# Optimization experiments

Hardware: AMD Instinct MI355X
Metric: run time of the kernel (lower is better)

## Reference

```python
import jax, jax.numpy as jnp
import numpy as np

K, NC, NA = 9, 13, 5
NB, NH, NW = 128, 26, 26
NT, L = 50, 2 * K + 3
NOOBJ, OBJ, SIL = 1.0, 5.0, 0.6
COORD_S, CLASS_S = 1.0, 1.0
PRETRAIN_EPOCHS = 15
TH, SHARP = 80.0, 2.0                      # corner-conf distance threshold (px), sharpness
SCALE = np.array([640.0, 480.0], np.float32)  # im_width, im_height used by corner_confidences
CONF0 = float(np.exp(SHARP) - 1.0)
ANCHORS = np.array([1.482, 2.2412, 2.0501, 3.1265, 2.3946, 4.6891,
                    3.1018, 3.991, 3.4879, 5.8851], np.float32).reshape(NA, 2)


def setup_inputs():
    k1, k2 = jax.random.split(jax.random.key(0))
    output = jax.random.normal(k1, (NB, NA * (2 * K + 1 + NC), NH, NW), dtype=jnp.float32)
    target = jax.random.uniform(k2, (NB, NT * L), dtype=jnp.float32)
    return {"output": output, "target": target, "epoch": 20}


def _corner_conf(pred, gt):
    # pred, gt: [..., K, 2] normalized corners -> mean per-corner confidence [...]
    d = jnp.sqrt((((pred - gt) * jnp.asarray(SCALE)) ** 2).sum(-1))  # pixel distance [..., K]
    c = (jnp.exp(SHARP * (1.0 - d / TH)) - 1.0) / CONF0
    return jnp.where(d < TH, c, 0.0).mean(-1)


def _region_loss(output, target, epoch):
    nAnch, nPix = NA * NH * NW, NH * NW
    tgt = jax.lax.stop_gradient(target).reshape(NB, NT, L)
    out = output.reshape(NB, NA, 2 * K + 1 + NC, NH, NW)
    # keypoint 0 gets sigmoid, the rest are raw offsets
    xs = jnp.concatenate([jax.nn.sigmoid(out[:, :, 0:1]), out[:, :, 2:2 * K:2]], axis=2)  # [B,A,K,H,W]
    ys = jnp.concatenate([jax.nn.sigmoid(out[:, :, 1:2]), out[:, :, 3:2 * K:2]], axis=2)
    conf = jax.nn.sigmoid(out[:, :, 2 * K])                             # [B,A,H,W]
    cls_logits = jnp.transpose(out[:, :, 2 * K + 1:], (0, 1, 3, 4, 2))  # [B,A,H,W,NC]

    gxg = jnp.arange(NW, dtype=jnp.float32)
    gyg = jnp.arange(NH, dtype=jnp.float32)
    px = (jax.lax.stop_gradient(xs) + gxg) / NW            # detached, as torch uses .data
    py = (jax.lax.stop_gradient(ys) + gyg[:, None]) / NH
    # pred corners per anchor cell, flat anchor index = a*H*W + j*W + i -> [B, A*H*W, K, 2]
    pc = jnp.transpose(jnp.stack([px, py], -1), (0, 1, 3, 4, 2, 5)).reshape(NB, nAnch, K, 2)

    gt_xy = tgt[:, :, 1:1 + 2 * K].reshape(NB, NT, K, 2)
    # torch loop breaks at first target with x1 == 0 -> cumulative validity
    valid = jnp.cumprod((tgt[:, :, 1] != 0).astype(jnp.int32), axis=1) > 0  # [B,T]

    # pass 1: max corner confidence over valid GT, per anchor cell
    def max_conf_step(cur, inp):
        gt_t, v_t = inp                                    # [B,K,2], [B]
        c = _corner_conf(pc, gt_t[:, None]).reshape(NB, NA, NH, NW)
        return jnp.where(v_t[:, None, None, None], jnp.maximum(cur, c), cur), None

    cur_confs, _ = jax.lax.scan(max_conf_step, jnp.zeros((NB, NA, NH, NW), jnp.float32),
                                (jnp.swapaxes(gt_xy, 0, 1), valid.T))
    conf_mask0 = jnp.where(cur_confs > SIL, 0.0, NOOBJ)

    # per-target quantities (vectorized over b,t)
    gx = gt_xy[..., 0] * NW                                # [B,T,K]
    gy = gt_xy[..., 1] * NH
    gi0 = jnp.clip(jnp.floor(gx[:, :, 0]).astype(jnp.int32), 0, NW - 1)  # [B,T]
    gj0 = jnp.clip(jnp.floor(gy[:, :, 0]).astype(jnp.int32), 0, NH - 1)
    # pred_box is fetched with best_n == -1 (as in the source); emulate torch negative flat index via mod
    flat_idx = jnp.mod(jnp.arange(NB)[:, None] * nAnch - nPix + gj0 * NW + gi0, NB * nAnch)
    pred_box = pc.reshape(NB * nAnch, K, 2)[flat_idx]      # [B,T,K,2]
    conf_t = _corner_conf(pred_box, gt_xy)                 # [B,T]
    gw = tgt[:, :, L - 2] * NW
    gh = tgt[:, :, L - 1] * NH
    aw, ah = ANCHORS[:, 0], ANCHORS[:, 1]
    mw = jnp.minimum(aw, gw[..., None])                    # centered-box IoU (bbox_iou, cxcywh)
    mh = jnp.minimum(ah, gh[..., None])
    inter = mw * mh
    iou = inter / (aw * ah + (gw * gh)[..., None] - inter)
    best_n = jnp.argmax(iou, axis=-1).astype(jnp.int32)    # [B,T] (first max, like strict '>')
    txv = gx - gi0[..., None].astype(jnp.float32)          # [B,T,K]
    tyv = gy - gj0[..., None].astype(jnp.float32)
    tclsv = tgt[:, :, 0]

    # pass 2: sequential scatter matching torch overwrite order over t
    barange = jnp.arange(NB)
    z = jnp.zeros((NB, NA, NH, NW), jnp.float32)
    zk = jnp.zeros((NB, NA, NH, NW, K), jnp.float32)

    def scatter_step(carry, inp):
        cm, clm, cfm, tx, ty, tcf, tcl = carry
        v, bn, gj, gi, cft, txt, tyt, tct = inp
        idx = (barange, bn, gj, gi)
        vk = v[:, None]
        cm = cm.at[idx].set(jnp.where(v, 1.0, cm[idx]))
        clm = clm.at[idx].set(jnp.where(v, 1.0, clm[idx]))
        cfm = cfm.at[idx].set(jnp.where(v, OBJ, cfm[idx]))
        tx = tx.at[idx].set(jnp.where(vk, txt, tx[idx]))
        ty = ty.at[idx].set(jnp.where(vk, tyt, ty[idx]))
        tcf = tcf.at[idx].set(jnp.where(v, cft, tcf[idx]))
        tcl = tcl.at[idx].set(jnp.where(v, tct, tcl[idx]))
        return (cm, clm, cfm, tx, ty, tcf, tcl), None

    inps = (valid.T, best_n.T, gj0.T, gi0.T, conf_t.T,
            jnp.swapaxes(txv, 0, 1), jnp.swapaxes(tyv, 0, 1), tclsv.T)
    (coord_mask, cls_mask, conf_mask, tx, ty, tconf, tcls), _ = jax.lax.scan(
        scatter_step, (z, z, conf_mask0, zk, zk, z, z), inps)

    # losses
    xsT = jnp.transpose(xs, (0, 1, 3, 4, 2))               # [B,A,H,W,K]
    ysT = jnp.transpose(ys, (0, 1, 3, 4, 2))
    cmk = coord_mask[..., None]
    loss_x = 0.5 * COORD_S * jnp.sum(((xsT - tx) * cmk) ** 2)
    loss_y = 0.5 * COORD_S * jnp.sum(((ysT - ty) * cmk) ** 2)
    sq = jnp.sqrt(conf_mask)
    loss_conf = 0.5 * jnp.sum(((conf - tconf) * sq) ** 2)
    labels = jnp.clip(tcls.astype(jnp.int32), 0, NC - 1)
    ce = -jnp.take_along_axis(jax.nn.log_softmax(cls_logits, axis=-1),
                              labels[..., None], axis=-1)[..., 0]
    loss_cls = CLASS_S * jnp.sum(ce * cls_mask)
    loss = loss_x + loss_y + loss_cls
    if epoch > PRETRAIN_EPOCHS:
        loss = loss + loss_conf
    return loss


def reference(output, target, epoch):
    return _region_loss(output, target, epoch)
```

## Files before the change

### kernel.cpp

```cpp
#include <hip/hip_runtime.h>
#include <math.h>

#define KK     9
#define NCLS   13
#define NANC   5
#define NBB    128
#define NHH    26
#define NWW    26
#define NTT    50
#define LL     21
#define CHC    32
#define NPIX   676
#define NANCHT 3380
#define NCELLT 432640
#define GTS    20
#define MWPB   106

#define LOG2E_F   1.4426950408889634f
#define K1C       2.8853900817779268f
#define K2C       0.036067376022224085f
#define SXW       24.615384615384617f
#define SYH       18.461538461538463f
#define THRESH_S  43.500902934225507f
#define CONF_T_SCALE 0.017390849194407297f
#define OBJ_W     5.0f
#define EPOCH_PRETRAIN 15
#define BIGV      6.0e18f

#define CULL_H2   0.36f
#define HSCALE    0.03125f

typedef __attribute__((ext_vector_type(2))) float f2;
typedef __attribute__((ext_vector_type(2))) _Float16 h2;
typedef __attribute__((ext_vector_type(4))) unsigned int u4;

static __device__ __forceinline__ float fast_exp2(float x){
  return __builtin_amdgcn_exp2f(x);
}
static __device__ __forceinline__ float fast_sqrt(float x){
  return __builtin_amdgcn_sqrtf(x);
}
static __device__ __forceinline__ float sigmoidf_(float x){
  return 1.0f/(1.0f + fast_exp2(-LOG2E_F*x));
}

__constant__ float c_anch[10] = {1.482f,2.2412f,2.0501f,3.1265f,2.3946f,4.6891f,
                                 3.1018f,3.991f,3.4879f,5.8851f};


__global__ __launch_bounds__(64) void prep_kernel(const float* __restrict__ tgt,
                                                  float* __restrict__ gts_neg,
                                                  int* __restrict__ nvalid){
  int b = blockIdx.x;
  int t = threadIdx.x;
  const float* trow = tgt + (size_t)b*NTT*LL;
  float v1 = (t < NTT) ? trow[t*LL + 1] : 0.0f;
  unsigned long long mk = __ballot(t < NTT && v1 != 0.0f);
  int firstInvalid = __ffsll(~mk) - 1;
  if (t == 0) nvalid[b] = firstInvalid;
  for (int idx = t; idx < NTT*GTS; idx += 64){
    int tt = idx / GTS;
    int c  = idx - tt*GTS;
    float v;
    if (c == 9 || c == 19)      v = BIGV;
    else if (c < 9)             v = -(trow[tt*LL + 1 + 2*c] * 640.0f);
    else                        v = -(trow[tt*LL + 2 + 2*(c-10)] * 480.0f);
    gts_neg[(size_t)b*NTT*GTS + idx] = v;
  }
}

__global__ __launch_bounds__(256) void region_confmask_kernel(
    const float* __restrict__ outp, const float* __restrict__ gts_neg,
    const int* __restrict__ nvalid, unsigned int* __restrict__ maskw,
    double* __restrict__ partials){
  int b = blockIdx.y;
  int cell = blockIdx.x * blockDim.x + threadIdx.x;

  __shared__ float sgt[NTT*GTS] __attribute__((aligned(16)));
  __shared__ h2   sgth[NTT*12] __attribute__((aligned(16)));
  const float* g32 = gts_neg + (size_t)b*NTT*GTS;
  for (int idx = threadIdx.x; idx < NTT*GTS; idx += 256)
    sgt[idx] = g32[idx];
  for (int widx = threadIdx.x; widx < NTT*12; widx += 256){
    int tt = widx / 12, w = widx - tt*12;
    float a0 = BIGV, a1 = BIGV;
    if (w < 10){ a0 = g32[tt*GTS + 2*w]; a1 = g32[tt*GTS + 2*w + 1]; }
    h2 hh;
    hh.x = (_Float16)(a0 * HSCALE);
    hh.y = (_Float16)(a1 * HSCALE);
    sgth[widx] = hh;
  }
  __syncthreads();

  int m0 = 1;
  float contrib = 0.0f;
  if (cell < NANCHT){
    int a   = cell / NPIX;
    int rem = cell - a*NPIX;
    int j   = rem / NWW;
    int i   = rem - j*NWW;
    const float* base = outp + (((size_t)b*NANC + a)*CHC)*NPIX + rem;

    f2 Pxp[5], Pyp[5];
#pragma unroll
    for (int k = 0; k < KK; ++k){
      float rx = base[(2*k)*NPIX];
      float ry = base[(2*k+1)*NPIX];
      if (k == 0){ rx = sigmoidf_(rx); ry = sigmoidf_(ry); }
      Pxp[k>>1][k&1] = (rx + (float)i) * SXW;
      Pyp[k>>1][k&1] = (ry + (float)j) * SYH;
    }
    Pxp[4][1] = 0.0f; Pyp[4][1] = 0.0f;

    h2 Pxh[5], Pyh[5];
#pragma unroll
    for (int p = 0; p < 5; ++p){
      Pxh[p].x = (_Float16)(Pxp[p].x * HSCALE);
      Pxh[p].y = (_Float16)(Pxp[p].y * HSCALE);
      Pyh[p].x = (_Float16)(Pyp[p].x * HSCALE);
      Pyh[p].y = (_Float16)(Pyp[p].y * HSCALE);
    }

    int nv = nvalid[b];
    const _Float16 thh = (_Float16)CULL_H2;
    unsigned long long qbits = 0ull;
#pragma unroll 2
    for (int t = 0; t < nv; ++t){
      const u4* gh = (const u4*)(sgth + t*12);
      u4 q0 = gh[0], q1 = gh[1], q2 = gh[2];
      h2 Xa[5] = { __builtin_bit_cast(h2, q0.x), __builtin_bit_cast(h2, q0.y),
                   __builtin_bit_cast(h2, q0.z), __builtin_bit_cast(h2, q0.w),
                   __builtin_bit_cast(h2, q1.x) };
      h2 Ya[5] = { __builtin_bit_cast(h2, q1.y), __builtin_bit_cast(h2, q1.z),
                   __builtin_bit_cast(h2, q1.w), __builtin_bit_cast(h2, q2.x),
                   __builtin_bit_cast(h2, q2.y) };
      h2 m2 = {(_Float16)60000.0f, (_Float16)60000.0f};
#pragma unroll
      for (int p = 0; p < 5; ++p){
        h2 dx = Pxh[p] + Xa[p];
        h2 dy = Pyh[p] + Ya[p];
        h2 r  = __builtin_elementwise_fma(dy, dy, dx*dx);
        m2 = __builtin_elementwise_min(m2, r);
      }
      if (m2.x < thh || m2.y < thh) qbits |= (1ull << t);
    }

    if (__any(qbits != 0ull)){
      bool exc = false;
      while (qbits){
        int t = __ffsll((long long)qbits) - 1;
        qbits &= qbits - 1;
        const float* gg = sgt + t*GTS;
        float s = 0.0f;
#pragma unroll
        for (int k = 0; k < KK; ++k){
          float dx = Pxp[k>>1][k&1] + gg[k];
          float dy = Pyp[k>>1][k&1] + gg[10+k];
          float d  = fast_sqrt(fmaf(dy, dy, dx*dx));
          float e  = fast_exp2(fmaf(d, -K2C, K1C));
          s += fmaxf(e, 1.0f);
        }
        exc |= (s > THRESH_S);
      }
      if (exc) m0 = 0;
    }
    float cf = sigmoidf_(base[(2*KK)*NPIX]);
    contrib = m0 ? 0.5f*cf*cf : 0.0f;
  }

  unsigned long long mb = __ballot(m0 != 0);
  int lane = threadIdx.x & 63;
  int wavebase = blockIdx.x * 256 + (threadIdx.x & ~63);
  if ((lane & 31) == 0 && wavebase < NANCHT){
    unsigned int w = (lane == 0) ? (unsigned int)mb : (unsigned int)(mb >> 32);
    maskw[(size_t)b*MWPB + (wavebase >> 5) + (lane >> 5)] = w;
  }

#pragma unroll
  for (int o = 32; o > 0; o >>= 1) contrib += __shfl_xor(contrib, o, 64);
  __shared__ float wsum[4];
  int wid = threadIdx.x >> 6;
  if (lane == 0) wsum[wid] = contrib;
  __syncthreads();
  if (threadIdx.x == 0){
    double tot = (double)wsum[0] + (double)wsum[1] + (double)wsum[2] + (double)wsum[3];
    partials[blockIdx.y * gridDim.x + blockIdx.x] = tot;
  }
}

__global__ __launch_bounds__(64) void scatter_loss_kernel(
    const float* __restrict__ outp, const float* __restrict__ tgt,
    const int* __restrict__ nvalid, const unsigned int* __restrict__ maskw,
    double* __restrict__ bc_part){
  int b = blockIdx.x;
  int t = threadIdx.x;
  __shared__ int keys[NTT];
  int nv = nvalid[b];
  bool valid = (t < nv);

  int key = -1, gi0 = 0, gj0 = 0, bn = 0;
  float txv[KK], tyv[KK];
  float conf_t = 0.0f, tcls = 0.0f;

  if (t < NTT){
    const float* trow = tgt + ((size_t)b*NTT + t)*LL;
    tcls = trow[0];
    float gx0 = trow[1]*(float)NWW;
    float gy0 = trow[2]*(float)NHH;
    gi0 = min(max((int)floorf(gx0), 0), NWW-1);
    gj0 = min(max((int)floorf(gy0), 0), NHH-1);
#pragma unroll
    for (int k = 0; k < KK; ++k){
      txv[k] = trow[1+2*k]*(float)NWW - (float)gi0;
      tyv[k] = trow[2+2*k]*(float)NHH - (float)gj0;
    }
    float gw = trow[LL-2]*(float)NWW, gh = trow[LL-1]*(float)NHH;
    float best = -1.0f;
    for (int a = 0; a < NANC; ++a){
      float aw = c_anch[2*a], ah = c_anch[2*a+1];
      float inter = fminf(aw, gw) * fminf(ah, gh);
      float iou = inter / (aw*ah + gw*gh - inter);
      if (iou > best){ best = iou; bn = a; }
    }
    key = bn*NPIX + gj0*NWW + gi0;
    keys[t] = key;

    long f = (long)b*NANCHT - NPIX + gj0*NWW + gi0;
    if (f < 0) f += NCELLT;
    int bb  = (int)(f / NANCHT);
    int rr  = (int)(f - (long)bb*NANCHT);
    int aa  = rr / NPIX;
    int rr2 = rr - aa*NPIX;
    int jj  = rr2 / NWW;
    int ii  = rr2 - jj*NWW;
    const float* pbase = outp + (((size_t)bb*NANC + aa)*CHC)*NPIX + rr2;
    float s = 0.0f;
#pragma unroll
    for (int k = 0; k < KK; ++k){
      float rx = pbase[(2*k)*NPIX], ry = pbase[(2*k+1)*NPIX];
      if (k == 0){ rx = sigmoidf_(rx); ry = sigmoidf_(ry); }
      float Pxx = (rx + (float)ii)*SXW, Pyy = (ry + (float)jj)*SYH;
      float dx = Pxx - trow[1+2*k]*640.0f;
      float dy = Pyy - trow[2+2*k]*480.0f;
      float d  = fast_sqrt(fmaf(dy, dy, dx*dx));
      float e  = fast_exp2(fmaf(d, -K2C, K1C));
      s += fmaxf(e, 1.0f);
    }
    conf_t = (s - 9.0f) * CONF_T_SCALE;
  }
  __syncthreads();

  bool winner = valid;
  if (valid){
    for (int u = t+1; u < nv; ++u) if (keys[u] == key){ winner = false; break; }
  }

  double lx = 0.0, ly = 0.0, lcls = 0.0, lcf = 0.0;
  if (winner){
    const float* cbase = outp + (((size_t)b*NANC + bn)*CHC)*NPIX + gj0*NWW + gi0;
    float sx = 0.0f, sy = 0.0f;
#pragma unroll
    for (int k = 0; k < KK; ++k){
      float rx = cbase[(2*k)*NPIX], ry = cbase[(2*k+1)*NPIX];
      if (k == 0){ rx = sigmoidf_(rx); ry = sigmoidf_(ry); }
      float dx = rx - txv[k], dy = ry - tyv[k];
      sx = fmaf(dx, dx, sx); sy = fmaf(dy, dy, sy);
    }
    lx = 0.5*(double)sx; ly = 0.5*(double)sy;

    float lg[NCLS], mx = -1e30f;
#pragma unroll
    for (int c = 0; c < NCLS; ++c){ lg[c] = cbase[(2*KK+1+c)*NPIX]; mx = fmaxf(mx, lg[c]); }
    float se = 0.0f;
#pragma unroll
    for (int c = 0; c < NCLS; ++c) se += fast_exp2((lg[c]-mx)*LOG2E_F);
    int label = min(max((int)tcls, 0), NCLS-1);
    lcls = (double)(mx + logf(se) - lg[label]);

    float cf = sigmoidf_(cbase[(2*KK)*NPIX]);
    int idx = bn*NPIX + gj0*NWW + gi0;
    int m0 = (maskw[(size_t)b*MWPB + (idx >> 5)] >> (idx & 31)) & 1;
    float dcf = cf - conf_t;
    lcf = 0.5*OBJ_W*(double)(dcf*dcf) - (m0 ? 0.5*(double)(cf*cf) : 0.0);
  }

#pragma unroll
  for (int o = 32; o > 0; o >>= 1){
    lx  += __shfl_xor(lx,  o, 64);
    ly  += __shfl_xor(ly,  o, 64);
    lcls+= __shfl_xor(lcls,o, 64);
    lcf += __shfl_xor(lcf, o, 64);
  }
  if (threadIdx.x == 0){
    double* bp = bc_part + (size_t)b*4;
    bp[0] = lx; bp[1] = ly; bp[2] = lcls; bp[3] = lcf;
  }
}

__global__ __launch_bounds__(256) void finalize_kernel(
    const double* __restrict__ bc_part, const double* __restrict__ partials,
    const int* __restrict__ epoch_p, float* __restrict__ outv){
  int tid = threadIdx.x;
  double vx=0, vy=0, vc=0, vf=0, vb=0;
  for (int i = tid; i < NBB; i += 256){
    vx += bc_part[4*i]; vy += bc_part[4*i+1];
    vc += bc_part[4*i+2]; vf += bc_part[4*i+3];
  }
  for (int i = tid; i < 14*NBB; i += 256) vb += partials[i];
#pragma unroll
  for (int o = 32; o > 0; o >>= 1){
    vx += __shfl_xor(vx, o, 64); vy += __shfl_xor(vy, o, 64);
    vc += __shfl_xor(vc, o, 64); vf += __shfl_xor(vf, o, 64);
    vb += __shfl_xor(vb, o, 64);
  }
  __shared__ double sm[5][4];
  int wid = tid >> 6, lane = tid & 63;
  if (lane == 0){ sm[0][wid]=vx; sm[1][wid]=vy; sm[2][wid]=vc; sm[3][wid]=vf; sm[4][wid]=vb; }
  __syncthreads();
  if (tid == 0){
    double fx=0, fy=0, fc=0, ff=0, fb=0;
    for (int w = 0; w < 4; ++w){ fx+=sm[0][w]; fy+=sm[1][w]; fc+=sm[2][w]; ff+=sm[3][w]; fb+=sm[4][w]; }
    double loss = fx + fy + fc;
    if (*epoch_p > EPOCH_PRETRAIN) loss += ff + fb;
    outv[0] = (float)loss;
  }
}

extern "C" void kernel_launch(void* const* d_in, const int* in_sizes, int n_in,
                              void* d_out, int out_size, void* d_ws, size_t ws_size,
                              hipStream_t stream){
  (void)in_sizes; (void)n_in; (void)out_size; (void)ws_size;
  const float* outp = (const float*)d_in[0];
  const float* tgt  = (const float*)d_in[1];
  const int*   ep   = (const int*)d_in[2];
  float* outv = (float*)d_out;
  char* ws = (char*)d_ws;

  double* bc_part  = (double*)(ws);
  double* partials = (double*)(ws + 4096);
  float*  gts_neg  = (float*) (ws + 18432);
  int*    nvalid   = (int*)   (ws + 530432);
  unsigned int* maskw = (unsigned int*)(ws + 530944);

  prep_kernel<<<dim3(NBB), dim3(64), 0, stream>>>(tgt, gts_neg, nvalid);
  region_confmask_kernel<<<dim3(14, NBB), dim3(256), 0, stream>>>(outp, gts_neg, nvalid, maskw, partials);
  scatter_loss_kernel<<<dim3(NBB), dim3(64), 0, stream>>>(outp, tgt, nvalid, maskw, bc_part);
  finalize_kernel<<<dim3(1), dim3(256), 0, stream>>>(bc_part, partials, ep, outv);
}
```

Measured before the change: 134.5 us.

## Precompute fp16 GT table in prep and read it via scalar constant loads

After: 139.5 us. 3.8% more time.

```diff
diff --git a/kernel.cpp b/kernel.cpp
--- a/kernel.cpp
+++ b/kernel.cpp
@@ -1,5 +1,6 @@
 #include <hip/hip_runtime.h>
 #include <math.h>
+#include <stdint.h>
 
 #define KK     9
 #define NCLS   13
@@ -15,6 +16,7 @@
 #define NCELLT 432640
 #define GTS    20
 #define MWPB   106
+#define GTH_W  12
 
 #define LOG2E_F   1.4426950408889634f
 #define K1C       2.8853900817779268f
@@ -33,6 +35,7 @@
 typedef __attribute__((ext_vector_type(2))) float f2;
 typedef __attribute__((ext_vector_type(2))) _Float16 h2;
 typedef __attribute__((ext_vector_type(4))) unsigned int u4;
+typedef __attribute__((ext_vector_type(2))) unsigned int u2;
 
 static __device__ __forceinline__ float fast_exp2(float x){
   return __builtin_amdgcn_exp2f(x);
@@ -44,12 +47,20 @@
   return 1.0f/(1.0f + fast_exp2(-LOG2E_F*x));
 }
 
+static __device__ __forceinline__ u4 sload_u4(const unsigned int* p){
+  return *(const __attribute__((address_space(4))) u4*)(uintptr_t)p;
+}
+static __device__ __forceinline__ u2 sload_u2(const unsigned int* p){
+  return *(const __attribute__((address_space(4))) u2*)(uintptr_t)p;
+}
+
 __constant__ float c_anch[10] = {1.482f,2.2412f,2.0501f,3.1265f,2.3946f,4.6891f,
                                  3.1018f,3.991f,3.4879f,5.8851f};
 
 
 __global__ __launch_bounds__(64) void prep_kernel(const float* __restrict__ tgt,
                                                   float* __restrict__ gts_neg,
+                                                  unsigned int* __restrict__ gth,
                                                   int* __restrict__ nvalid){
   int b = blockIdx.x;
   int t = threadIdx.x;
@@ -67,106 +78,116 @@
     else                        v = -(trow[tt*LL + 2 + 2*(c-10)] * 480.0f);
     gts_neg[(size_t)b*NTT*GTS + idx] = v;
   }
+  for (int idx = t; idx < NTT*GTH_W; idx += 64){
+    int tt = idx / GTH_W;
+    int w  = idx - tt*GTH_W;
+    const float* tr2 = trow + tt*LL;
+    float a0 = BIGV, a1 = BIGV;
+    if (w < 5){
+      int k0 = 2*w;
+      a0 = -(tr2[1 + 2*k0] * 20.0f);
+      if (k0 + 1 < KK) a1 = -(tr2[1 + 2*(k0+1)] * 20.0f);
+    } else if (w < 10){
+      int k0 = 2*(w-5);
+      a0 = -(tr2[2 + 2*k0] * 15.0f);
+      if (k0 + 1 < KK) a1 = -(tr2[2 + 2*(k0+1)] * 15.0f);
+    }
+    h2 hh; hh.x = (_Float16)a0; hh.y = (_Float16)a1;
+    gth[(size_t)b*NTT*GTH_W + idx] = __builtin_bit_cast(unsigned int, hh);
+  }
 }
 
 __global__ __launch_bounds__(256) void region_confmask_kernel(
     const float* __restrict__ outp, const float* __restrict__ gts_neg,
+    const unsigned int* __restrict__ gth,
     const int* __restrict__ nvalid, unsigned int* __restrict__ maskw,
     double* __restrict__ partials){
   int b = blockIdx.y;
   int cell = blockIdx.x * blockDim.x + threadIdx.x;
+  bool live = (cell < NANCHT);
+  int cellc = live ? cell : (NANCHT-1);
 
   __shared__ float sgt[NTT*GTS] __attribute__((aligned(16)));
-  __shared__ h2   sgth[NTT*12] __attribute__((aligned(16)));
   const float* g32 = gts_neg + (size_t)b*NTT*GTS;
   for (int idx = threadIdx.x; idx < NTT*GTS; idx += 256)
     sgt[idx] = g32[idx];
-  for (int widx = threadIdx.x; widx < NTT*12; widx += 256){
-    int tt = widx / 12, w = widx - tt*12;
-    float a0 = BIGV, a1 = BIGV;
-    if (w < 10){ a0 = g32[tt*GTS + 2*w]; a1 = g32[tt*GTS + 2*w + 1]; }
-    h2 hh;
-    hh.x = (_Float16)(a0 * HSCALE);
-    hh.y = (_Float16)(a1 * HSCALE);
-    sgth[widx] = hh;
-  }
   __syncthreads();
 
+  int a   = cellc / NPIX;
+  int rem = cellc - a*NPIX;
+  int j   = rem / NWW;
+  int i   = rem - j*NWW;
+  const float* base = outp + (((size_t)b*NANC + a)*CHC)*NPIX + rem;
+
+  f2 Pxp[5], Pyp[5];
+#pragma unroll
+  for (int k = 0; k < KK; ++k){
+    float rx = base[(2*k)*NPIX];
+    float ry = base[(2*k+1)*NPIX];
+    if (k == 0){ rx = sigmoidf_(rx); ry = sigmoidf_(ry); }
+    Pxp[k>>1][k&1] = (rx + (float)i) * SXW;
+    Pyp[k>>1][k&1] = (ry + (float)j) * SYH;
+  }
+  Pxp[4][1] = 0.0f; Pyp[4][1] = 0.0f;
+
+  h2 Pxh[5], Pyh[5];
+#pragma unroll
+  for (int p = 0; p < 5; ++p){
+    Pxh[p].x = (_Float16)(Pxp[p].x * HSCALE);
+    Pxh[p].y = (_Float16)(Pxp[p].y * HSCALE);
+    Pyh[p].x = (_Float16)(Pyp[p].x * HSCALE);
+    Pyh[p].y = (_Float16)(Pyp[p].y * HSCALE);
+  }
+
+  int nv = nvalid[b];
+  const unsigned int* gthb = gth + (size_t)b*NTT*GTH_W;
+  const _Float16 thh = (_Float16)CULL_H2;
+  unsigned long long qbits = 0ull;
+#pragma unroll 2
+  for (int t = 0; t < nv; ++t){
+    u4 q0 = sload_u4(gthb + t*GTH_W);
+    u4 q1 = sload_u4(gthb + t*GTH_W + 4);
+    u2 q2 = sload_u2(gthb + t*GTH_W + 8);
+    h2 Xa[5] = { __builtin_bit_cast(h2, q0.x), __builtin_bit_cast(h2, q0.y),
+                 __builtin_bit_cast(h2, q0.z), __builtin_bit_cast(h2, q0.w),
+                 __builtin_bit_cast(h2, q1.x) };
+    h2 Ya[5] = { __builtin_bit_cast(h2, q1.y), __builtin_bit_cast(h2, q1.z),
+                 __builtin_bit_cast(h2, q1.w), __builtin_bit_cast(h2, q2.x),
+                 __builtin_bit_cast(h2, q2.y) };
+    h2 m2 = {(_Float16)60000.0f, (_Float16)60000.0f};
+#pragma unroll
+    for (int p = 0; p < 5; ++p){
+      h2 dx = Pxh[p] + Xa[p];
+      h2 dy = Pyh[p] + Ya[p];
+      h2 r  = __builtin_elementwise_fma(dy, dy, dx*dx);
+      m2 = __builtin_elementwise_min(m2, r);
+    }
+    _Float16 mm = (m2.x < m2.y) ? m2.x : m2.y;
+    if (mm < thh) qbits |= (1ull << t);
+  }
+
   int m0 = 1;
-  float contrib = 0.0f;
-  if (cell < NANCHT){
-    int a   = cell / NPIX;
-    int rem = cell - a*NPIX;
-    int j   = rem / NWW;
-    int i   = rem - j*NWW;
-    const float* base = outp + (((size_t)b*NANC + a)*CHC)*NPIX + rem;
-
-    f2 Pxp[5], Pyp[5];
-#pragma unroll
-    for (int k = 0; k < KK; ++k){
-      float rx = base[(2*k)*NPIX];
-      float ry = base[(2*k+1)*NPIX];
-      if (k == 0){ rx = sigmoidf_(rx); ry = sigmoidf_(ry); }
-      Pxp[k>>1][k&1] = (rx + (float)i) * SXW;
-      Pyp[k>>1][k&1] = (ry + (float)j) * SYH;
-    }
-    Pxp[4][1] = 0.0f; Pyp[4][1] = 0.0f;
-
-    h2 Pxh[5], Pyh[5];
-#pragma unroll
-    for (int p = 0; p < 5; ++p){
-      Pxh[p].x = (_Float16)(Pxp[p].x * HSCALE);
-      Pxh[p].y = (_Float16)(Pxp[p].y * HSCALE);
-      Pyh[p].x = (_Float16)(Pyp[p].x * HSCALE);
-      Pyh[p].y = (_Float16)(Pyp[p].y * HSCALE);
-    }
-
-    int nv = nvalid[b];
-    const _Float16 thh = (_Float16)CULL_H2;
-    unsigned long long qbits = 0ull;
-#pragma unroll 2
-    for (int t = 0; t < nv; ++t){
-      const u4* gh = (const u4*)(sgth + t*12);
-      u4 q0 = gh[0], q1 = gh[1], q2 = gh[2];
-      h2 Xa[5] = { __builtin_bit_cast(h2, q0.x), __builtin_bit_cast(h2, q0.y),
-                   __builtin_bit_cast(h2, q0.z), __builtin_bit_cast(h2, q0.w),
-                   __builtin_bit_cast(h2, q1.x) };
-      h2 Ya[5] = { __builtin_bit_cast(h2, q1.y), __builtin_bit_cast(h2, q1.z),
-                   __builtin_bit_cast(h2, q1.w), __builtin_bit_cast(h2, q2.x),
-                   __builtin_bit_cast(h2, q2.y) };
-      h2 m2 = {(_Float16)60000.0f, (_Float16)60000.0f};
-#pragma unroll
-      for (int p = 0; p < 5; ++p){
-        h2 dx = Pxh[p] + Xa[p];
-        h2 dy = Pyh[p] + Ya[p];
-        h2 r  = __builtin_elementwise_fma(dy, dy, dx*dx);
-        m2 = __builtin_elementwise_min(m2, r);
+  if (__any(qbits != 0ull)){
+    bool exc = false;
+    while (qbits){
+      int t = __ffsll((long long)qbits) - 1;
+      qbits &= qbits - 1;
+      const float* gg = sgt + t*GTS;
+      float s = 0.0f;
+#pragma unroll
+      for (int k = 0; k < KK; ++k){
+        float dx = Pxp[k>>1][k&1] + gg[k];
+        float dy = Pyp[k>>1][k&1] + gg[10+k];
+        float d  = fast_sqrt(fmaf(dy, dy, dx*dx));
+        float e  = fast_exp2(fmaf(d, -K2C, K1C));
+        s += fmaxf(e, 1.0f);
       }
-      if (m2.x < thh || m2.y < thh) qbits |= (1ull << t);
-    }
-
-    if (__any(qbits != 0ull)){
-      bool exc = false;
-      while (qbits){
-        int t = __ffsll((long long)qbits) - 1;
-        qbits &= qbits - 1;
-        const float* gg = sgt + t*GTS;
-        float s = 0.0f;
-#pragma unroll
-        for (int k = 0; k < KK; ++k){
-          float dx = Pxp[k>>1][k&1] + gg[k];
-          float dy = Pyp[k>>1][k&1] + gg[10+k];
-          float d  = fast_sqrt(fmaf(dy, dy, dx*dx));
-          float e  = fast_exp2(fmaf(d, -K2C, K1C));
-          s += fmaxf(e, 1.0f);
-        }
-        exc |= (s > THRESH_S);
-      }
-      if (exc) m0 = 0;
-    }
-    float cf = sigmoidf_(base[(2*KK)*NPIX]);
-    contrib = m0 ? 0.5f*cf*cf : 0.0f;
-  }
+      exc |= (s > THRESH_S);
+    }
+    if (exc) m0 = 0;
+  }
+  float cf = sigmoidf_(base[(2*KK)*NPIX]);
+  float contrib = (m0 && live) ? 0.5f*cf*cf : 0.0f;
 
   unsigned long long mb = __ballot(m0 != 0);
   int lane = threadIdx.x & 63;
@@ -341,9 +362,10 @@
   float*  gts_neg  = (float*) (ws + 18432);
   int*    nvalid   = (int*)   (ws + 530432);
   unsigned int* maskw = (unsigned int*)(ws + 530944);
-
-  prep_kernel<<<dim3(NBB), dim3(64), 0, stream>>>(tgt, gts_neg, nvalid);
-  region_confmask_kernel<<<dim3(14, NBB), dim3(256), 0, stream>>>(outp, gts_neg, nvalid, maskw, partials);
+  unsigned int* gth   = (unsigned int*)(ws + 585216);
+
+  prep_kernel<<<dim3(NBB), dim3(64), 0, stream>>>(tgt, gts_neg, gth, nvalid);
+  region_confmask_kernel<<<dim3(14, NBB), dim3(256), 0, stream>>>(outp, gts_neg, gth, nvalid, maskw, partials);
   scatter_loss_kernel<<<dim3(NBB), dim3(64), 0, stream>>>(outp, tgt, nvalid, maskw, bc_part);
   finalize_kernel<<<dim3(1), dim3(256), 0, stream>>>(bc_part, partials, ep, outv);
 }
```
